# Kernel tuning notes

Hardware: AMD Instinct MI355X
Metric: run time of the kernel (lower is better)

Reference implementation:

```python
import jax, jax.numpy as jnp
import numpy as np

B, N, D = 4, 2048, 256
H = 8
HD = D // H
FF = 1024
EPS = 1e-5


def layer_norm(x, g, b):
    mu = jnp.mean(x, axis=-1, keepdims=True)
    var = jnp.mean((x - mu) ** 2, axis=-1, keepdims=True)
    return (x - mu) * jax.lax.rsqrt(var + EPS) * g + b


def setup_inputs() -> dict:
    key = jax.random.key(0)
    ks = jax.random.split(key, 12)
    s = 0.02
    return {
        "tokens": jax.random.normal(ks[0], (B, N, D), dtype=jnp.float32),
        "key_padding_mask": jnp.zeros((B, N), dtype=bool),
        "ln1_g": jnp.ones((D,), jnp.float32),
        "ln1_b": jnp.zeros((D,), jnp.float32),
        "wq": jax.random.normal(ks[1], (D, D), jnp.float32) * s,
        "bq": jnp.zeros((D,), jnp.float32),
        "wk": jax.random.normal(ks[2], (D, D), jnp.float32) * s,
        "bk": jnp.zeros((D,), jnp.float32),
        "wv": jax.random.normal(ks[3], (D, D), jnp.float32) * s,
        "bv": jnp.zeros((D,), jnp.float32),
        "wo": jax.random.normal(ks[4], (D, D), jnp.float32) * s,
        "bo": jnp.zeros((D,), jnp.float32),
        "ln2_g": jnp.ones((D,), jnp.float32),
        "ln2_b": jnp.zeros((D,), jnp.float32),
        "w1": jax.random.normal(ks[5], (D, FF), jnp.float32) * s,
        "b1": jnp.zeros((FF,), jnp.float32),
        "w2": jax.random.normal(ks[6], (FF, D), jnp.float32) * s,
        "b2": jnp.zeros((D,), jnp.float32),
    }


def reference(tokens, key_padding_mask, ln1_g, ln1_b, wq, bq, wk, bk, wv, bv,
              wo, bo, ln2_g, ln2_b, w1, b1, w2, b2):
    x = tokens
    # --- self-attention sublayer (pre-LN) ---
    xn = layer_norm(x, ln1_g, ln1_b)
    q = (xn @ wq + bq).reshape(B, N, H, HD).transpose(0, 2, 1, 3)  # [B,H,N,HD]
    k = (xn @ wk + bk).reshape(B, N, H, HD).transpose(0, 2, 1, 3)
    v = (xn @ wv + bv).reshape(B, N, H, HD).transpose(0, 2, 1, 3)
    scores = jnp.einsum('bhqd,bhkd->bhqk', q, k) / np.sqrt(HD).astype(np.float32)
    scores = jnp.where(key_padding_mask[:, None, None, :], -jnp.inf, scores)
    probs = jax.nn.softmax(scores, axis=-1)
    attn = jnp.einsum('bhqk,bhkd->bhqd', probs, v)
    attn = attn.transpose(0, 2, 1, 3).reshape(B, N, D)
    x = x + (attn @ wo + bo)
    # --- feed-forward sublayer (pre-LN) ---
    xn2 = layer_norm(x, ln2_g, ln2_b)
    h = jax.nn.gelu(xn2 @ w1 + b1, approximate=False)  # torch GELU is exact erf
    x = x + (h @ w2 + b2)
    return x
```

## Files before the change

### kernel.cpp

```cpp
#include <hip/hip_runtime.h>
#include <cmath>

typedef __attribute__((ext_vector_type(8))) __bf16 bf16x8;
typedef __attribute__((ext_vector_type(4))) __bf16 bf16x4;
typedef __attribute__((ext_vector_type(4))) float  f32x4;

constexpr int NB   = 4;
constexpr int SEQ  = 2048;
constexpr int DM   = 256;
constexpr int NH   = 8;
constexpr int DH   = 32;
constexpr int DFF  = 1024;
constexpr int MTOK = NB * SEQ;

__global__ __launch_bounds__(256) void ln_kernel(const float* __restrict__ x,
                                                 const float* __restrict__ g,
                                                 const float* __restrict__ b,
                                                 __bf16* __restrict__ out) {
  int wave = threadIdx.x >> 6, lane = threadIdx.x & 63;
  int row = blockIdx.x * 4 + wave;
  const float* xr = x + (size_t)row * DM;
  f32x4 v = *(const f32x4*)(xr + lane * 4);
  float s  = v[0] + v[1] + v[2] + v[3];
  float sq = v[0]*v[0] + v[1]*v[1] + v[2]*v[2] + v[3]*v[3];
  #pragma unroll
  for (int off = 1; off < 64; off <<= 1) {
    s  += __shfl_xor(s, off);
    sq += __shfl_xor(sq, off);
  }
  float mu  = s * (1.0f / DM);
  float var = sq * (1.0f / DM) - mu * mu;
  float rs  = rsqrtf(var + 1e-5f);
  f32x4 gv = *(const f32x4*)(g + lane * 4);
  f32x4 bv = *(const f32x4*)(b + lane * 4);
  bf16x4 o;
  #pragma unroll
  for (int i = 0; i < 4; ++i) o[i] = (__bf16)((v[i] - mu) * rs * gv[i] + bv[i]);
  *(bf16x4*)(out + (size_t)row * DM + lane * 4) = o;
}

__global__ __launch_bounds__(256) void prep_kernel(
    const float* __restrict__ wq, const float* __restrict__ wk, const float* __restrict__ wv,
    const float* __restrict__ wo, const float* __restrict__ w1, const float* __restrict__ w2,
    const unsigned char* __restrict__ mask, const float* __restrict__ tokens,
    const float* __restrict__ ln1g, const float* __restrict__ ln1b,
    __bf16* __restrict__ wqkvT, __bf16* __restrict__ woT,
    __bf16* __restrict__ w1T, __bf16* __restrict__ w2T,
    float* __restrict__ madd_g, __bf16* __restrict__ xn1) {
  __shared__ float tile[32][33];
  int bid = blockIdx.x;
  int tid = threadIdx.x;
  if (bid >= 800) {
    int row = (bid - 800) * 4 + (tid >> 6);
    int lane = tid & 63;
    const float* xr = tokens + (size_t)row * DM;
    f32x4 v = *(const f32x4*)(xr + lane * 4);
    float s  = v[0] + v[1] + v[2] + v[3];
    float sq = v[0]*v[0] + v[1]*v[1] + v[2]*v[2] + v[3]*v[3];
    #pragma unroll
    for (int off = 1; off < 64; off <<= 1) {
      s  += __shfl_xor(s, off);
      sq += __shfl_xor(sq, off);
    }
    float mu  = s * (1.0f / DM);
    float var = sq * (1.0f / DM) - mu * mu;
    float rs  = rsqrtf(var + 1e-5f);
    f32x4 gv = *(const f32x4*)(ln1g + lane * 4);
    f32x4 bv = *(const f32x4*)(ln1b + lane * 4);
    bf16x4 o;
    #pragma unroll
    for (int i = 0; i < 4; ++i) o[i] = (__bf16)((v[i] - mu) * rs * gv[i] + bv[i]);
    *(bf16x4*)(xn1 + (size_t)row * DM + lane * 4) = o;
    return;
  }
  if (bid >= 768) {
    int idx = (bid - 768) * 256 + tid;
    madd_g[idx] = mask[idx] ? -__builtin_inff() : 0.0f;
    return;
  }
  const float* W; __bf16* Wt; int K, N, n0, k0;
  if (bid < 256) {
    int z = bid >> 6, local = bid & 63;
    K = 256; N = 256;
    n0 = (local & 7) * 32; k0 = (local >> 3) * 32;
    if      (z == 0) { W = wq; Wt = wqkvT;          }
    else if (z == 1) { W = wk; Wt = wqkvT + 65536;  }
    else if (z == 2) { W = wv; Wt = wqkvT + 131072; }
    else             { W = wo; Wt = woT;            }
  } else if (bid < 512) {
    int local = bid - 256;
    W = w1; Wt = w1T; K = 256; N = 1024;
    n0 = (local & 31) * 32; k0 = (local >> 5) * 32;
  } else {
    int local = bid - 512;
    W = w2; Wt = w2T; K = 1024; N = 256;
    n0 = (local & 7) * 32; k0 = (local >> 3) * 32;
  }
  {
    int kl = tid >> 3, n4 = (tid & 7) * 4;
    f32x4 v = *(const f32x4*)(W + (size_t)(k0 + kl) * N + n0 + n4);
    tile[kl][n4 + 0] = v[0]; tile[kl][n4 + 1] = v[1];
    tile[kl][n4 + 2] = v[2]; tile[kl][n4 + 3] = v[3];
  }
  __syncthreads();
  {
    int nl = tid >> 3, k4 = (tid & 7) * 4;
    bf16x4 o;
    #pragma unroll
    for (int i = 0; i < 4; ++i) o[i] = (__bf16)tile[k4 + i][nl];
    *(bf16x4*)(Wt + (size_t)(n0 + nl) * K + k0 + k4) = o;
  }
}

template<int BM, int BN, int EP>
__global__ __launch_bounds__(256) void gemm_bt(
    const __bf16* __restrict__ A, const __bf16* __restrict__ Bt,
    int M, int N, int K,
    const float* __restrict__ bias,
    const float* __restrict__ bq, const float* __restrict__ bk, const float* __restrict__ bv,
    const float* __restrict__ resid, float* __restrict__ outf,
    __bf16* __restrict__ outb,
    __bf16* __restrict__ outq, __bf16* __restrict__ outk, __bf16* __restrict__ outv) {
  constexpr int MT = BM / 32, NT = BN / 32;
  constexpr int AP = BM / 32, BP = BN / 32;
  __shared__ __bf16 As[BM * 64];
  __shared__ __bf16 Bs[BN * 64];
  int tid = threadIdx.x;
  int wave = tid >> 6, lane = tid & 63;
  int wm = wave >> 1, wn = wave & 1;
  int quad = lane >> 4, l16 = lane & 15;
  int m0 = blockIdx.x * BM, n0 = blockIdx.y * BN;
  int lrow = lane >> 3;
  int lcg  = ((lane & 7) ^ lrow) * 8;

  f32x4 acc[MT][NT];
  #pragma unroll
  for (int mt = 0; mt < MT; ++mt)
    #pragma unroll
    for (int nt = 0; nt < NT; ++nt)
      #pragma unroll
      for (int r = 0; r < 4; ++r) acc[mt][nt][r] = 0.0f;

  bf16x8 ap[AP], bp[BP];
  #pragma unroll
  for (int i = 0; i < AP; ++i) {
    int rbase = wave * (BM / 4) + i * 8;
    ap[i] = *(const bf16x8*)(A + (size_t)(m0 + rbase + lrow) * K + lcg);
  }
  #pragma unroll
  for (int i = 0; i < BP; ++i) {
    int rbase = wave * (BN / 4) + i * 8;
    bp[i] = *(const bf16x8*)(Bt + (size_t)(n0 + rbase + lrow) * K + lcg);
  }
  #pragma unroll
  for (int i = 0; i < AP; ++i) {
    int rbase = wave * (BM / 4) + i * 8;
    *(bf16x8*)&As[rbase * 64 + lane * 8] = ap[i];
  }
  #pragma unroll
  for (int i = 0; i < BP; ++i) {
    int rbase = wave * (BN / 4) + i * 8;
    *(bf16x8*)&Bs[rbase * 64 + lane * 8] = bp[i];
  }
  __syncthreads();

  for (int kt = 0; kt < K; kt += 64) {
    bool more = (kt + 64) < K;
    if (more) {
      #pragma unroll
      for (int i = 0; i < AP; ++i) {
        int rbase = wave * (BM / 4) + i * 8;
        ap[i] = *(const bf16x8*)(A + (size_t)(m0 + rbase + lrow) * K + kt + 64 + lcg);
      }
      #pragma unroll
      for (int i = 0; i < BP; ++i) {
        int rbase = wave * (BN / 4) + i * 8;
        bp[i] = *(const bf16x8*)(Bt + (size_t)(n0 + rbase + lrow) * K + kt + 64 + lcg);
      }
    }
    #pragma unroll
    for (int ks = 0; ks < 2; ++ks) {
      bf16x8 af[MT], bfr[NT];
      #pragma unroll
      for (int mt = 0; mt < MT; ++mt) {
        int row = wm * (BM / 2) + mt * 16 + l16;
        af[mt] = *(const bf16x8*)&As[row * 64 + (((ks * 4 + quad) ^ (l16 & 7)) * 8)];
      }
      #pragma unroll
      for (int nt = 0; nt < NT; ++nt) {
        int row = wn * (BN / 2) + nt * 16 + l16;
        bfr[nt] = *(const bf16x8*)&Bs[row * 64 + (((ks * 4 + quad) ^ (l16 & 7)) * 8)];
      }
      #pragma unroll
      for (int mt = 0; mt < MT; ++mt)
        #pragma unroll
        for (int nt = 0; nt < NT; ++nt)
          acc[mt][nt] = __builtin_amdgcn_mfma_f32_16x16x32_bf16(af[mt], bfr[nt], acc[mt][nt], 0, 0, 0);
    }
    if (more) {
      __syncthreads();
      #pragma unroll
      for (int i = 0; i < AP; ++i) {
        int rbase = wave * (BM / 4) + i * 8;
        *(bf16x8*)&As[rbase * 64 + lane * 8] = ap[i];
      }
      #pragma unroll
      for (int i = 0; i < BP; ++i) {
        int rbase = wave * (BN / 4) + i * 8;
        *(bf16x8*)&Bs[rbase * 64 + lane * 8] = bp[i];
      }
      __syncthreads();
    }
  }

  #pragma unroll
  for (int mt = 0; mt < MT; ++mt)
  #pragma unroll
  for (int nt = 0; nt < NT; ++nt)
  #pragma unroll
  for (int r = 0; r < 4; ++r) {
    int gm = m0 + wm * (BM / 2) + mt * 16 + quad * 4 + r;
    int gn = n0 + wn * (BN / 2) + nt * 16 + l16;
    float v = acc[mt][nt][r];
    if constexpr (EP == 0) {
      int which = gn >> 8, nn = gn & 255;
      const float* bp2 = which == 0 ? bq : (which == 1 ? bk : bv);
      v += bp2[nn];
      int h = nn >> 5, hd = nn & 31;
      int bb = gm >> 11, tok = gm & 2047;
      if (which == 2) {
        outv[(((size_t)(bb * NH + h)) * DH + hd) * SEQ + tok] = (__bf16)v;
      } else {
        __bf16* dst = which == 0 ? outq : outk;
        dst[(((size_t)(bb * NH + h)) * SEQ + tok) * DH + hd] = (__bf16)v;
      }
    } else if constexpr (EP == 1) {
      v += bias[gn] + resid[(size_t)gm * N + gn];
      outf[(size_t)gm * N + gn] = v;
    } else {
      v += bias[gn];
      float v2 = v * v;
      float t = __builtin_amdgcn_exp2f(v * (2.3022082f + 0.10294324f * v2));
      outb[(size_t)gm * N + gn] = (__bf16)(v * t * __builtin_amdgcn_rcpf(t + 1.0f));
    }
  }
}

__global__ __launch_bounds__(64) void attn_kernel(
    const __bf16* __restrict__ Q, const __bf16* __restrict__ K,
    const __bf16* __restrict__ Vt, const float* __restrict__ madd_g,
    __bf16* __restrict__ out) {
  constexpr float C2 = 0.2550350030061664f;
  constexpr int NT = SEQ / 64;
  __shared__ __bf16 Ps[2][2][16][72];
  int bh = blockIdx.x;
  int qw = blockIdx.y * 32;
  int b  = bh >> 3, h = bh & 7;
  int lane = threadIdx.x & 63;
  int quad = lane >> 4, l16 = lane & 15;
  const __bf16* Qb = Q  + (size_t)bh * SEQ * DH;
  const __bf16* Kb = K  + (size_t)bh * SEQ * DH;
  const __bf16* Vb = Vt + (size_t)bh * DH * SEQ;
  const float* maddb = madd_g + b * SEQ;

  bf16x8 qf[2];
  #pragma unroll
  for (int qg = 0; qg < 2; ++qg)
    qf[qg] = *(const bf16x8*)(Qb + (size_t)(qw + qg * 16 + l16) * DH + quad * 8);

  bf16x8 ones;
  #pragma unroll
  for (int i = 0; i < 8; ++i) ones[i] = (__bf16)1.0f;

  f32x4 o[2][2], ol[2];
  #pragma unroll
  for (int qg = 0; qg < 2; ++qg) {
    #pragma unroll
    for (int nt = 0; nt < 2; ++nt)
      #pragma unroll
      for (int r = 0; r < 4; ++r) o[qg][nt][r] = 0.0f;
    #pragma unroll
    for (int r = 0; r < 4; ++r) ol[qg][r] = 0.0f;
  }

  f32x4 zf; zf[0] = zf[1] = zf[2] = zf[3] = 0.0f;

  {
    f32x4 s[2][4];
    #pragma unroll
    for (int mt = 0; mt < 4; ++mt) {
      bf16x8 kf = *(const bf16x8*)(Kb + (size_t)(mt * 16 + l16) * DH + quad * 8);
      s[0][mt] = __builtin_amdgcn_mfma_f32_16x16x32_bf16(kf, qf[0], zf, 0, 0, 0);
      s[1][mt] = __builtin_amdgcn_mfma_f32_16x16x32_bf16(kf, qf[1], zf, 0, 0, 0);
    }
    #pragma unroll
    for (int mt = 0; mt < 4; ++mt) {
      f32x4 md = *(const f32x4*)(maddb + mt * 16 + quad * 4);
      #pragma unroll
      for (int qg = 0; qg < 2; ++qg) {
        bf16x4 pv;
        #pragma unroll
        for (int r = 0; r < 4; ++r)
          pv[r] = (__bf16)__builtin_amdgcn_exp2f(fmaf(s[qg][mt][r], C2, md[r]));
        *(bf16x4*)&Ps[0][qg][l16][mt * 16 + quad * 4] = pv;
      }
    }
  }

  int buf = 0;
  for (int kt = 0; kt < NT; ++kt) {
    int k0 = kt * 64;
    bool more = (kt + 1) < NT;

    bf16x8 kf[4];
    if (more) {
      #pragma unroll
      for (int mt = 0; mt < 4; ++mt)
        kf[mt] = *(const bf16x8*)(Kb + (size_t)(k0 + 64 + mt * 16 + l16) * DH + quad * 8);
    }
    bf16x8 vf[2][2];
    #pragma unroll
    for (int ks = 0; ks < 2; ++ks)
      #pragma unroll
      for (int nt = 0; nt < 2; ++nt)
        vf[ks][nt] = *(const bf16x8*)(Vb + (size_t)(nt * 16 + l16) * SEQ + k0 + ks * 32 + quad * 8);
    bf16x8 pf[2][2];
    #pragma unroll
    for (int ks = 0; ks < 2; ++ks)
      #pragma unroll
      for (int qg = 0; qg < 2; ++qg)
        pf[ks][qg] = *(const bf16x8*)&Ps[buf][qg][l16][ks * 32 + quad * 8];

    #pragma unroll
    for (int ks = 0; ks < 2; ++ks)
      #pragma unroll
      for (int qg = 0; qg < 2; ++qg) {
        #pragma unroll
        for (int nt = 0; nt < 2; ++nt)
          o[qg][nt] = __builtin_amdgcn_mfma_f32_16x16x32_bf16(pf[ks][qg], vf[ks][nt], o[qg][nt], 0, 0, 0);
        ol[qg] = __builtin_amdgcn_mfma_f32_16x16x32_bf16(pf[ks][qg], ones, ol[qg], 0, 0, 0);
      }

    if (more) {
      f32x4 s[2][4];
      #pragma unroll
      for (int mt = 0; mt < 4; ++mt) {
        s[0][mt] = __builtin_amdgcn_mfma_f32_16x16x32_bf16(kf[mt], qf[0], zf, 0, 0, 0);
        s[1][mt] = __builtin_amdgcn_mfma_f32_16x16x32_bf16(kf[mt], qf[1], zf, 0, 0, 0);
      }
      #pragma unroll
      for (int mt = 0; mt < 4; ++mt) {
        f32x4 md = *(const f32x4*)(maddb + k0 + 64 + mt * 16 + quad * 4);
        #pragma unroll
        for (int qg = 0; qg < 2; ++qg) {
          bf16x4 pv;
          #pragma unroll
          for (int r = 0; r < 4; ++r)
            pv[r] = (__bf16)__builtin_amdgcn_exp2f(fmaf(s[qg][mt][r], C2, md[r]));
          *(bf16x4*)&Ps[buf ^ 1][qg][l16][mt * 16 + quad * 4] = pv;
        }
      }
    }
    buf ^= 1;
  }

  #pragma unroll
  for (int qg = 0; qg < 2; ++qg) {
    f32x4 inv;
    #pragma unroll
    for (int r = 0; r < 4; ++r) inv[r] = 1.0f / ol[qg][r];
    #pragma unroll
    for (int nt = 0; nt < 2; ++nt)
      #pragma unroll
      for (int r = 0; r < 4; ++r) {
        int q   = qw + qg * 16 + quad * 4 + r;
        int col = h * DH + nt * 16 + l16;
        out[((size_t)(b * SEQ + q)) * DM + col] = (__bf16)(o[qg][nt][r] * inv[r]);
      }
  }
}

extern "C" void kernel_launch(void* const* d_in, const int* in_sizes, int n_in,
                              void* d_out, int out_size, void* d_ws, size_t ws_size,
                              hipStream_t stream) {
  const float* tokens = (const float*)d_in[0];
  const unsigned char* mask = (const unsigned char*)d_in[1];
  const float* ln1g = (const float*)d_in[2];
  const float* ln1b = (const float*)d_in[3];
  const float* wq = (const float*)d_in[4];
  const float* bq = (const float*)d_in[5];
  const float* wk = (const float*)d_in[6];
  const float* bk = (const float*)d_in[7];
  const float* wv = (const float*)d_in[8];
  const float* bv = (const float*)d_in[9];
  const float* wo = (const float*)d_in[10];
  const float* bo = (const float*)d_in[11];
  const float* ln2g = (const float*)d_in[12];
  const float* ln2b = (const float*)d_in[13];
  const float* w1 = (const float*)d_in[14];
  const float* b1 = (const float*)d_in[15];
  const float* w2 = (const float*)d_in[16];
  const float* b2 = (const float*)d_in[17];
  float* out = (float*)d_out;
  char* ws = (char*)d_ws;

  __bf16* wqkvT = (__bf16*)(ws + 0);
  __bf16* woT   = (__bf16*)(ws + 393216);
  __bf16* w1T   = (__bf16*)(ws + 524288);
  __bf16* w2T   = (__bf16*)(ws + 1048576);
  __bf16* xn1   = (__bf16*)(ws + 1572864);
  __bf16* qb    = (__bf16*)(ws + 5767168);
  __bf16* kb    = (__bf16*)(ws + 9961472);
  __bf16* vt    = (__bf16*)(ws + 18350080);
  __bf16* attn  = (__bf16*)(ws + 22544384);
  float*  x1    = (float*)(ws + 26738688);
  __bf16* xn2   = (__bf16*)(ws + 35127296);
  __bf16* hbuf  = (__bf16*)(ws + 39321600);
  float*  madd  = (float*)(ws + 56098816);

  prep_kernel<<<2848, 256, 0, stream>>>(
      wq, wk, wv, wo, w1, w2, mask, tokens, ln1g, ln1b,
      wqkvT, woT, w1T, w2T, madd, xn1);

  gemm_bt<128, 128, 0><<<dim3(64, 6), 256, 0, stream>>>(
      xn1, wqkvT, MTOK, 768, 256, nullptr, bq, bk, bv,
      nullptr, nullptr, nullptr, qb, kb, vt);

  attn_kernel<<<dim3(32, SEQ / 32), 64, 0, stream>>>(qb, kb, vt, madd, attn);

  gemm_bt<64, 64, 1><<<dim3(128, 4), 256, 0, stream>>>(
      attn, woT, MTOK, 256, 256, bo, nullptr, nullptr, nullptr,
      tokens, x1, nullptr, nullptr, nullptr, nullptr);

  ln_kernel<<<MTOK / 4, 256, 0, stream>>>(x1, ln2g, ln2b, xn2);

  gemm_bt<128, 128, 2><<<dim3(64, 8), 256, 0, stream>>>(
      xn2, w1T, MTOK, DFF, 256, b1, nullptr, nullptr, nullptr,
      nullptr, nullptr, hbuf, nullptr, nullptr, nullptr);

  gemm_bt<64, 64, 1><<<dim3(128, 4), 256, 0, stream>>>(
      hbuf, w2T, MTOK, 256, DFF, b2, nullptr, nullptr, nullptr,
      x1, out, nullptr, nullptr, nullptr, nullptr);
}
```

Before: 209.2 us.

## Split attention over two key halves and combine partials in a reduce kernel

The attention kernel now splits the key sequence into two halves via a third grid dimension, doubling the number of workgroups. Each half writes unnormalized fp32 partial outputs and row sums into workspace buffers that alias xn1 and hbuf, which are dead at this point. A new reduce kernel adds the two partials, normalizes, and writes the bf16 attention output. This relies on the fixed exponent with no running max, so partials combine by plain addition. The gain in occupancy for a small-grid attention kernel is paid for with extra fp32 traffic and one more launch.

Measured after the change: 212.5 us. No clear change (+1.6%).

```diff
diff --git a/kernel.cpp b/kernel.cpp
--- a/kernel.cpp
+++ b/kernel.cpp
@@ -249,12 +249,13 @@
 __global__ __launch_bounds__(64) void attn_kernel(
     const __bf16* __restrict__ Q, const __bf16* __restrict__ K,
     const __bf16* __restrict__ Vt, const float* __restrict__ madd_g,
-    __bf16* __restrict__ out) {
+    float* __restrict__ Opart, float* __restrict__ lpart) {
   constexpr float C2 = 0.2550350030061664f;
-  constexpr int NT = SEQ / 64;
+  constexpr int HT = SEQ / 128;
   __shared__ __bf16 Ps[2][2][16][72];
   int bh = blockIdx.x;
   int qw = blockIdx.y * 32;
+  int half = blockIdx.z;
   int b  = bh >> 3, h = bh & 7;
   int lane = threadIdx.x & 63;
   int quad = lane >> 4, l16 = lane & 15;
@@ -262,6 +263,7 @@
   const __bf16* Kb = K  + (size_t)bh * SEQ * DH;
   const __bf16* Vb = Vt + (size_t)bh * DH * SEQ;
   const float* maddb = madd_g + b * SEQ;
+  int kbase = half * (SEQ / 2);
 
   bf16x8 qf[2];
   #pragma unroll
@@ -289,13 +291,13 @@
     f32x4 s[2][4];
     #pragma unroll
     for (int mt = 0; mt < 4; ++mt) {
-      bf16x8 kf = *(const bf16x8*)(Kb + (size_t)(mt * 16 + l16) * DH + quad * 8);
+      bf16x8 kf = *(const bf16x8*)(Kb + (size_t)(kbase + mt * 16 + l16) * DH + quad * 8);
       s[0][mt] = __builtin_amdgcn_mfma_f32_16x16x32_bf16(kf, qf[0], zf, 0, 0, 0);
       s[1][mt] = __builtin_amdgcn_mfma_f32_16x16x32_bf16(kf, qf[1], zf, 0, 0, 0);
     }
     #pragma unroll
     for (int mt = 0; mt < 4; ++mt) {
-      f32x4 md = *(const f32x4*)(maddb + mt * 16 + quad * 4);
+      f32x4 md = *(const f32x4*)(maddb + kbase + mt * 16 + quad * 4);
       #pragma unroll
       for (int qg = 0; qg < 2; ++qg) {
         bf16x4 pv;
@@ -308,9 +310,9 @@
   }
 
   int buf = 0;
-  for (int kt = 0; kt < NT; ++kt) {
-    int k0 = kt * 64;
-    bool more = (kt + 1) < NT;
+  for (int kt = 0; kt < HT; ++kt) {
+    int k0 = kbase + kt * 64;
+    bool more = (kt + 1) < HT;
 
     bf16x8 kf[4];
     if (more) {
@@ -364,20 +366,42 @@
     buf ^= 1;
   }
 
+  float* Op = Opart + (size_t)half * MTOK * DM;
   #pragma unroll
   for (int qg = 0; qg < 2; ++qg) {
-    f32x4 inv;
-    #pragma unroll
-    for (int r = 0; r < 4; ++r) inv[r] = 1.0f / ol[qg][r];
     #pragma unroll
     for (int nt = 0; nt < 2; ++nt)
       #pragma unroll
       for (int r = 0; r < 4; ++r) {
         int q   = qw + qg * 16 + quad * 4 + r;
         int col = h * DH + nt * 16 + l16;
-        out[((size_t)(b * SEQ + q)) * DM + col] = (__bf16)(o[qg][nt][r] * inv[r]);
-      }
-  }
+        Op[((size_t)(b * SEQ + q)) * DM + col] = o[qg][nt][r];
+      }
+    if (l16 == 0) {
+      #pragma unroll
+      for (int r = 0; r < 4; ++r)
+        lpart[((((size_t)half * NB + b) * NH) + h) * SEQ + qw + qg * 16 + quad * 4 + r] = ol[qg][r];
+    }
+  }
+}
+
+__global__ __launch_bounds__(256) void reduce_kernel(const float* __restrict__ Opart,
+                                                     const float* __restrict__ lpart,
+                                                     __bf16* __restrict__ out) {
+  int wave = threadIdx.x >> 6, lane = threadIdx.x & 63;
+  int row = blockIdx.x * 4 + wave;
+  int b = row >> 11, tok = row & 2047;
+  int c4 = lane * 4;
+  int h = c4 >> 5;
+  float l = lpart[((size_t)b * NH + h) * SEQ + tok] +
+            lpart[(((size_t)NB + b) * NH + h) * SEQ + tok];
+  float inv = 1.0f / l;
+  f32x4 a0 = *(const f32x4*)(Opart + (size_t)row * DM + c4);
+  f32x4 a1 = *(const f32x4*)(Opart + (size_t)MTOK * DM + (size_t)row * DM + c4);
+  bf16x4 o;
+  #pragma unroll
+  for (int i = 0; i < 4; ++i) o[i] = (__bf16)((a0[i] + a1[i]) * inv);
+  *(bf16x4*)(out + (size_t)row * DM + c4) = o;
 }
 
 extern "C" void kernel_launch(void* const* d_in, const int* in_sizes, int n_in,
@@ -409,6 +433,7 @@
   __bf16* w1T   = (__bf16*)(ws + 524288);
   __bf16* w2T   = (__bf16*)(ws + 1048576);
   __bf16* xn1   = (__bf16*)(ws + 1572864);
+  float*  lpart = (float*)(ws + 1572864);
   __bf16* qb    = (__bf16*)(ws + 5767168);
   __bf16* kb    = (__bf16*)(ws + 9961472);
   __bf16* vt    = (__bf16*)(ws + 18350080);
@@ -416,7 +441,9 @@
   float*  x1    = (float*)(ws + 26738688);
   __bf16* xn2   = (__bf16*)(ws + 35127296);
   __bf16* hbuf  = (__bf16*)(ws + 39321600);
+  float*  Opart = (float*)(ws + 39321600);
   float*  madd  = (float*)(ws + 56098816);
+
 
   prep_kernel<<<2848, 256, 0, stream>>>(
       wq, wk, wv, wo, w1, w2, mask, tokens, ln1g, ln1b,
@@ -426,7 +453,9 @@
       xn1, wqkvT, MTOK, 768, 256, nullptr, bq, bk, bv,
       nullptr, nullptr, nullptr, qb, kb, vt);
 
-  attn_kernel<<<dim3(32, SEQ / 32), 64, 0, stream>>>(qb, kb, vt, madd, attn);
+  attn_kernel<<<dim3(32, SEQ / 32, 2), 64, 0, stream>>>(qb, kb, vt, madd, Opart, lpart);
+
+  reduce_kernel<<<MTOK / 4, 256, 0, stream>>>(Opart, lpart, attn);
 
   gemm_bt<64, 64, 1><<<dim3(128, 4), 256, 0, stream>>>(
       attn, woT, MTOK, 256, 256, bo, nullptr, nullptr, nullptr,
```

## Split attention keys across two blocks and fuse partial combine into Wo GEMM

Applied to the files above, without the earlier changes.

Attention now runs 256-thread blocks of four waves, each wave handling 16 queries. K and V tiles are staged in shared memory and shared across the waves, and the key range is split in two halves along a new grid dimension (split-K). Each half writes unnormalized fp32 partial outputs and row sums. The output projection GEMM combines the two halves, normalizes and converts to bf16 while loading its A tile. The QKV GEMM tile also changes to 128x64 to launch more blocks. This aims for more parallelism and K/V reuse, at the cost of extra fp32 traffic for the partials.

Result: faster. 200.2 us (-4.3%).

```diff
diff --git a/kernel.cpp b/kernel.cpp
--- a/kernel.cpp
+++ b/kernel.cpp
@@ -112,7 +112,7 @@
   }
 }
 
-template<int BM, int BN, int EP>
+template<int BM, int BN, int EP, int AF = 0>
 __global__ __launch_bounds__(256) void gemm_bt(
     const __bf16* __restrict__ A, const __bf16* __restrict__ Bt,
     int M, int N, int K,
@@ -120,7 +120,8 @@
     const float* __restrict__ bq, const float* __restrict__ bk, const float* __restrict__ bv,
     const float* __restrict__ resid, float* __restrict__ outf,
     __bf16* __restrict__ outb,
-    __bf16* __restrict__ outq, __bf16* __restrict__ outk, __bf16* __restrict__ outv) {
+    __bf16* __restrict__ outq, __bf16* __restrict__ outk, __bf16* __restrict__ outv,
+    const float* __restrict__ Af = nullptr, const float* __restrict__ lpart = nullptr) {
   constexpr int MT = BM / 32, NT = BN / 32;
   constexpr int AP = BM / 32, BP = BN / 32;
   __shared__ __bf16 As[BM * 64];
@@ -133,6 +134,29 @@
   int lrow = lane >> 3;
   int lcg  = ((lane & 7) ^ lrow) * 8;
 
+  auto loadA = [&](int rbase, int kcol) -> bf16x8 {
+    int gr = m0 + rbase + lrow;
+    if constexpr (AF == 0) {
+      return *(const bf16x8*)(A + (size_t)gr * K + kcol);
+    } else {
+      const float* p0 = Af + (size_t)gr * K + kcol;
+      const float* p1 = p0 + (size_t)MTOK * DM;
+      f32x4 a0 = *(const f32x4*)p0, a0b = *(const f32x4*)(p0 + 4);
+      f32x4 a1 = *(const f32x4*)p1, a1b = *(const f32x4*)(p1 + 4);
+      int bb = gr >> 11, tok = gr & 2047, hh = kcol >> 5;
+      float l = lpart[((size_t)bb * NH + hh) * SEQ + tok] +
+                lpart[(((size_t)NB + bb) * NH + hh) * SEQ + tok];
+      float inv = 1.0f / l;
+      bf16x8 o;
+      #pragma unroll
+      for (int i = 0; i < 4; ++i) {
+        o[i]     = (__bf16)((a0[i]  + a1[i])  * inv);
+        o[i + 4] = (__bf16)((a0b[i] + a1b[i]) * inv);
+      }
+      return o;
+    }
+  };
+
   f32x4 acc[MT][NT];
   #pragma unroll
   for (int mt = 0; mt < MT; ++mt)
@@ -143,10 +167,7 @@
 
   bf16x8 ap[AP], bp[BP];
   #pragma unroll
-  for (int i = 0; i < AP; ++i) {
-    int rbase = wave * (BM / 4) + i * 8;
-    ap[i] = *(const bf16x8*)(A + (size_t)(m0 + rbase + lrow) * K + lcg);
-  }
+  for (int i = 0; i < AP; ++i) ap[i] = loadA(wave * (BM / 4) + i * 8, lcg);
   #pragma unroll
   for (int i = 0; i < BP; ++i) {
     int rbase = wave * (BN / 4) + i * 8;
@@ -168,10 +189,7 @@
     bool more = (kt + 64) < K;
     if (more) {
       #pragma unroll
-      for (int i = 0; i < AP; ++i) {
-        int rbase = wave * (BM / 4) + i * 8;
-        ap[i] = *(const bf16x8*)(A + (size_t)(m0 + rbase + lrow) * K + kt + 64 + lcg);
-      }
+      for (int i = 0; i < AP; ++i) ap[i] = loadA(wave * (BM / 4) + i * 8, kt + 64 + lcg);
       #pragma unroll
       for (int i = 0; i < BP; ++i) {
         int rbase = wave * (BN / 4) + i * 8;
@@ -246,137 +264,103 @@
   }
 }
 
-__global__ __launch_bounds__(64) void attn_kernel(
+__global__ __launch_bounds__(256) void attn_kernel(
     const __bf16* __restrict__ Q, const __bf16* __restrict__ K,
     const __bf16* __restrict__ Vt, const float* __restrict__ madd_g,
-    __bf16* __restrict__ out) {
+    float* __restrict__ Opart, float* __restrict__ lpart) {
   constexpr float C2 = 0.2550350030061664f;
-  constexpr int NT = SEQ / 64;
-  __shared__ __bf16 Ps[2][2][16][72];
+  __shared__ __bf16 Ks[128][36];
+  __shared__ __bf16 Vs[32][132];
+  __shared__ __bf16 Ps[4][16][68];
   int bh = blockIdx.x;
-  int qw = blockIdx.y * 32;
+  int q0 = blockIdx.y * 64;
+  int half = blockIdx.z;
   int b  = bh >> 3, h = bh & 7;
-  int lane = threadIdx.x & 63;
+  int tid = threadIdx.x;
+  int wave = tid >> 6, lane = tid & 63;
   int quad = lane >> 4, l16 = lane & 15;
   const __bf16* Qb = Q  + (size_t)bh * SEQ * DH;
   const __bf16* Kb = K  + (size_t)bh * SEQ * DH;
   const __bf16* Vb = Vt + (size_t)bh * DH * SEQ;
   const float* maddb = madd_g + b * SEQ;
-
-  bf16x8 qf[2];
-  #pragma unroll
-  for (int qg = 0; qg < 2; ++qg)
-    qf[qg] = *(const bf16x8*)(Qb + (size_t)(qw + qg * 16 + l16) * DH + quad * 8);
+  int qw = q0 + wave * 16;
+  int kbase = half * (SEQ / 2);
+
+  bf16x8 qf = *(const bf16x8*)(Qb + (size_t)(qw + l16) * DH + quad * 8);
 
   bf16x8 ones;
   #pragma unroll
   for (int i = 0; i < 8; ++i) ones[i] = (__bf16)1.0f;
 
-  f32x4 o[2][2], ol[2];
-  #pragma unroll
-  for (int qg = 0; qg < 2; ++qg) {
-    #pragma unroll
-    for (int nt = 0; nt < 2; ++nt)
-      #pragma unroll
-      for (int r = 0; r < 4; ++r) o[qg][nt][r] = 0.0f;
-    #pragma unroll
-    for (int r = 0; r < 4; ++r) ol[qg][r] = 0.0f;
-  }
+  f32x4 o[2], ol;
+  #pragma unroll
+  for (int nt = 0; nt < 2; ++nt)
+    #pragma unroll
+    for (int r = 0; r < 4; ++r) o[nt][r] = 0.0f;
+  #pragma unroll
+  for (int r = 0; r < 4; ++r) ol[r] = 0.0f;
 
   f32x4 zf; zf[0] = zf[1] = zf[2] = zf[3] = 0.0f;
 
-  {
-    f32x4 s[2][4];
-    #pragma unroll
-    for (int mt = 0; mt < 4; ++mt) {
-      bf16x8 kf = *(const bf16x8*)(Kb + (size_t)(mt * 16 + l16) * DH + quad * 8);
-      s[0][mt] = __builtin_amdgcn_mfma_f32_16x16x32_bf16(kf, qf[0], zf, 0, 0, 0);
-      s[1][mt] = __builtin_amdgcn_mfma_f32_16x16x32_bf16(kf, qf[1], zf, 0, 0, 0);
-    }
-    #pragma unroll
-    for (int mt = 0; mt < 4; ++mt) {
-      f32x4 md = *(const f32x4*)(maddb + mt * 16 + quad * 4);
-      #pragma unroll
-      for (int qg = 0; qg < 2; ++qg) {
+  for (int st = 0; st < 8; ++st) {
+    int kb0 = kbase + st * 128;
+    __syncthreads();
+    #pragma unroll
+    for (int p = 0; p < 2; ++p) {
+      int c = p * 256 + tid, row = c >> 2, cg = (c & 3) * 8;
+      *(bf16x8*)&Ks[row][cg] = *(const bf16x8*)(Kb + (size_t)(kb0 + row) * DH + cg);
+    }
+    #pragma unroll
+    for (int p = 0; p < 2; ++p) {
+      int c = p * 256 + tid, row = c >> 4, cg = (c & 15) * 8;
+      *(bf16x8*)&Vs[row][cg] = *(const bf16x8*)(Vb + (size_t)row * SEQ + kb0 + cg);
+    }
+    __syncthreads();
+
+    #pragma unroll
+    for (int sub = 0; sub < 2; ++sub) {
+      int kl = sub * 64;
+      f32x4 s[4];
+      #pragma unroll
+      for (int mt = 0; mt < 4; ++mt) {
+        bf16x8 kf = *(const bf16x8*)&Ks[kl + mt * 16 + l16][quad * 8];
+        s[mt] = __builtin_amdgcn_mfma_f32_16x16x32_bf16(kf, qf, zf, 0, 0, 0);
+      }
+      #pragma unroll
+      for (int mt = 0; mt < 4; ++mt) {
+        f32x4 md = *(const f32x4*)(maddb + kb0 + kl + mt * 16 + quad * 4);
         bf16x4 pv;
         #pragma unroll
         for (int r = 0; r < 4; ++r)
-          pv[r] = (__bf16)__builtin_amdgcn_exp2f(fmaf(s[qg][mt][r], C2, md[r]));
-        *(bf16x4*)&Ps[0][qg][l16][mt * 16 + quad * 4] = pv;
-      }
-    }
-  }
-
-  int buf = 0;
-  for (int kt = 0; kt < NT; ++kt) {
-    int k0 = kt * 64;
-    bool more = (kt + 1) < NT;
-
-    bf16x8 kf[4];
-    if (more) {
-      #pragma unroll
-      for (int mt = 0; mt < 4; ++mt)
-        kf[mt] = *(const bf16x8*)(Kb + (size_t)(k0 + 64 + mt * 16 + l16) * DH + quad * 8);
-    }
-    bf16x8 vf[2][2];
-    #pragma unroll
-    for (int ks = 0; ks < 2; ++ks)
-      #pragma unroll
-      for (int nt = 0; nt < 2; ++nt)
-        vf[ks][nt] = *(const bf16x8*)(Vb + (size_t)(nt * 16 + l16) * SEQ + k0 + ks * 32 + quad * 8);
-    bf16x8 pf[2][2];
-    #pragma unroll
-    for (int ks = 0; ks < 2; ++ks)
-      #pragma unroll
-      for (int qg = 0; qg < 2; ++qg)
-        pf[ks][qg] = *(const bf16x8*)&Ps[buf][qg][l16][ks * 32 + quad * 8];
-
-    #pragma unroll
-    for (int ks = 0; ks < 2; ++ks)
-      #pragma unroll
-      for (int qg = 0; qg < 2; ++qg) {
+          pv[r] = (__bf16)__builtin_amdgcn_exp2f(fmaf(s[mt][r], C2, md[r]));
+        *(bf16x4*)&Ps[wave][l16][mt * 16 + quad * 4] = pv;
+      }
+      #pragma unroll
+      for (int ks = 0; ks < 2; ++ks) {
+        bf16x8 pf = *(const bf16x8*)&Ps[wave][l16][ks * 32 + quad * 8];
         #pragma unroll
-        for (int nt = 0; nt < 2; ++nt)
-          o[qg][nt] = __builtin_amdgcn_mfma_f32_16x16x32_bf16(pf[ks][qg], vf[ks][nt], o[qg][nt], 0, 0, 0);
-        ol[qg] = __builtin_amdgcn_mfma_f32_16x16x32_bf16(pf[ks][qg], ones, ol[qg], 0, 0, 0);
-      }
-
-    if (more) {
-      f32x4 s[2][4];
-      #pragma unroll
-      for (int mt = 0; mt < 4; ++mt) {
-        s[0][mt] = __builtin_amdgcn_mfma_f32_16x16x32_bf16(kf[mt], qf[0], zf, 0, 0, 0);
-        s[1][mt] = __builtin_amdgcn_mfma_f32_16x16x32_bf16(kf[mt], qf[1], zf, 0, 0, 0);
-      }
-      #pragma unroll
-      for (int mt = 0; mt < 4; ++mt) {
-        f32x4 md = *(const f32x4*)(maddb + k0 + 64 + mt * 16 + quad * 4);
-        #pragma unroll
-        for (int qg = 0; qg < 2; ++qg) {
-          bf16x4 pv;
-          #pragma unroll
-          for (int r = 0; r < 4; ++r)
-            pv[r] = (__bf16)__builtin_amdgcn_exp2f(fmaf(s[qg][mt][r], C2, md[r]));
-          *(bf16x4*)&Ps[buf ^ 1][qg][l16][mt * 16 + quad * 4] = pv;
+        for (int nt = 0; nt < 2; ++nt) {
+          bf16x8 vf = *(const bf16x8*)&Vs[nt * 16 + l16][kl + ks * 32 + quad * 8];
+          o[nt] = __builtin_amdgcn_mfma_f32_16x16x32_bf16(pf, vf, o[nt], 0, 0, 0);
         }
-      }
-    }
-    buf ^= 1;
-  }
-
-  #pragma unroll
-  for (int qg = 0; qg < 2; ++qg) {
-    f32x4 inv;
-    #pragma unroll
-    for (int r = 0; r < 4; ++r) inv[r] = 1.0f / ol[qg][r];
-    #pragma unroll
-    for (int nt = 0; nt < 2; ++nt)
-      #pragma unroll
-      for (int r = 0; r < 4; ++r) {
-        int q   = qw + qg * 16 + quad * 4 + r;
-        int col = h * DH + nt * 16 + l16;
-        out[((size_t)(b * SEQ + q)) * DM + col] = (__bf16)(o[qg][nt][r] * inv[r]);
-      }
+        ol = __builtin_amdgcn_mfma_f32_16x16x32_bf16(pf, ones, ol, 0, 0, 0);
+      }
+    }
+  }
+
+  float* Op = Opart + (size_t)half * MTOK * DM;
+  #pragma unroll
+  for (int nt = 0; nt < 2; ++nt)
+    #pragma unroll
+    for (int r = 0; r < 4; ++r) {
+      int q   = qw + quad * 4 + r;
+      int col = h * DH + nt * 16 + l16;
+      Op[((size_t)(b * SEQ + q)) * DM + col] = o[nt][r];
+    }
+  if (l16 == 0) {
+    #pragma unroll
+    for (int r = 0; r < 4; ++r)
+      lpart[((((size_t)half * NB + b) * NH) + h) * SEQ + qw + quad * 4 + r] = ol[r];
   }
 }
 
@@ -409,28 +393,29 @@
   __bf16* w1T   = (__bf16*)(ws + 524288);
   __bf16* w2T   = (__bf16*)(ws + 1048576);
   __bf16* xn1   = (__bf16*)(ws + 1572864);
+  float*  lpart = (float*)(ws + 1572864);
   __bf16* qb    = (__bf16*)(ws + 5767168);
   __bf16* kb    = (__bf16*)(ws + 9961472);
   __bf16* vt    = (__bf16*)(ws + 18350080);
-  __bf16* attn  = (__bf16*)(ws + 22544384);
   float*  x1    = (float*)(ws + 26738688);
   __bf16* xn2   = (__bf16*)(ws + 35127296);
   __bf16* hbuf  = (__bf16*)(ws + 39321600);
+  float*  Opart = (float*)(ws + 39321600);
   float*  madd  = (float*)(ws + 56098816);
 
   prep_kernel<<<2848, 256, 0, stream>>>(
       wq, wk, wv, wo, w1, w2, mask, tokens, ln1g, ln1b,
       wqkvT, woT, w1T, w2T, madd, xn1);
 
-  gemm_bt<128, 128, 0><<<dim3(64, 6), 256, 0, stream>>>(
+  gemm_bt<128, 64, 0><<<dim3(64, 12), 256, 0, stream>>>(
       xn1, wqkvT, MTOK, 768, 256, nullptr, bq, bk, bv,
       nullptr, nullptr, nullptr, qb, kb, vt);
 
-  attn_kernel<<<dim3(32, SEQ / 32), 64, 0, stream>>>(qb, kb, vt, madd, attn);
-
-  gemm_bt<64, 64, 1><<<dim3(128, 4), 256, 0, stream>>>(
-      attn, woT, MTOK, 256, 256, bo, nullptr, nullptr, nullptr,
-      tokens, x1, nullptr, nullptr, nullptr, nullptr);
+  attn_kernel<<<dim3(32, SEQ / 64, 2), 256, 0, stream>>>(qb, kb, vt, madd, Opart, lpart);
+
+  gemm_bt<64, 64, 1, 1><<<dim3(128, 4), 256, 0, stream>>>(
+      nullptr, woT, MTOK, 256, 256, bo, nullptr, nullptr, nullptr,
+      tokens, x1, nullptr, nullptr, nullptr, nullptr, Opart, lpart);
 
   ln_kernel<<<MTOK / 4, 256, 0, stream>>>(x1, ln2g, ln2b, xn2);
 
```
